# Kernel tuning notes

Measured on AMD Instinct MI355X. Metric: run time of the kernel, lower is better.

## Reference

```python
import jax, jax.numpy as jnp
import numpy as np

B, S, H, A = 64, 2048, 512, 512

def setup_inputs() -> dict:
    key = jax.random.key(0)
    k = jax.random.split(key, 8)
    s = 1.0 / np.sqrt(H)
    sa = 1.0 / np.sqrt(A)
    return {
        "decoder_output": jax.random.normal(k[0], (B, H), jnp.float32),
        "encoder_output": jax.random.normal(k[1], (B, S, H), jnp.float32),
        "W_dec": jax.random.uniform(k[2], (A, H), jnp.float32, -s, s),
        "b_dec": jax.random.uniform(k[3], (A,), jnp.float32, -s, s),
        "W_enc": jax.random.uniform(k[4], (A, H), jnp.float32, -s, s),
        "b_enc": jax.random.uniform(k[5], (A,), jnp.float32, -s, s),
        "V": jax.random.uniform(k[6], (1, A), jnp.float32, -sa, sa),
        "b_v": jax.random.uniform(k[7], (1,), jnp.float32, -sa, sa),
    }

def reference(decoder_output, encoder_output, W_dec, b_dec, W_enc, b_enc, V, b_v):
    # dec proj: (B, A); enc proj: (B, S, A)
    dec_p = decoder_output @ W_dec.T + b_dec
    enc_p = jnp.einsum('bsh,ah->bsa', encoder_output, W_enc) + b_enc
    h = jnp.tanh(dec_p[:, None, :] + enc_p)          # (B, S, A)
    scores = jnp.einsum('bsa,a->bs', h, V[0]) + b_v[0]  # (B, S)
    attn = jax.nn.softmax(scores, axis=-1)           # softmax over seq dim
    ctx = jnp.einsum('bs,bsh->bh', attn, encoder_output)  # (B, H)
    out = jnp.concatenate([ctx, decoder_output], axis=-1)  # (B, 2H)
    return out
```

## Files before the change

### kernel.cpp

```cpp
#include <hip/hip_runtime.h>
#include <cstdint>
#include <cstddef>

#define NB 64
#define NS 2048
#define NH 512
#define NA 512

#define BM 64
#define BK 32

typedef __attribute__((ext_vector_type(8))) short short8;
typedef __attribute__((ext_vector_type(4))) float f32x4;

__device__ inline short f2bf(float f) {
    union { float f; uint32_t u; } v; v.f = f;
    uint32_t u = v.u;
    uint32_t r = (u + 0x7fffu + ((u >> 16) & 1u)) >> 16;
    return (short)r;
}

__global__ __launch_bounds__(256) void k_decp(const float* __restrict__ dec,
                                              const float* __restrict__ Wd,
                                              const float* __restrict__ bd,
                                              const float* __restrict__ be,
                                              float* __restrict__ dp) {
    int b = blockIdx.x;
    __shared__ float dl[NH];
    for (int i = threadIdx.x; i < NH; i += 256) dl[i] = dec[b * NH + i];
    __syncthreads();
    for (int a = threadIdx.x; a < NA; a += 256) {
        const float4* wr = (const float4*)(Wd + (size_t)a * NH);
        float acc = 0.f;
#pragma unroll 8
        for (int h4 = 0; h4 < NH / 4; ++h4) {
            float4 w = wr[h4];
            acc += dl[h4*4+0]*w.x + dl[h4*4+1]*w.y + dl[h4*4+2]*w.z + dl[h4*4+3]*w.w;
        }
        dp[b * NA + a] = acc + bd[a] + be[a];
    }
}

__global__ __launch_bounds__(256) void k_packw(const float* __restrict__ We,
                                               short* __restrict__ wsw) {
    int t = blockIdx.x * 256 + threadIdx.x;
    int slot = t & 3;
    int a = (t >> 2) & (NA - 1);
    int kt = t >> 11;
    const float* src = We + (size_t)a * NH + kt * 32 + slot * 8;
    int dslot = slot ^ ((a >> 1) & 3);
    short* dst = wsw + (((size_t)kt * NA + a) * 4 + dslot) * 8;
    short8 o;
#pragma unroll
    for (int j = 0; j < 8; ++j) o[j] = f2bf(src[j]);
    *(short8*)dst = o;
}

__global__ __launch_bounds__(256, 2) void k_scores(const float* __restrict__ enc,
                                                   const short* __restrict__ wsw,
                                                   const float* __restrict__ dp,
                                                   const float* __restrict__ V,
                                                   float* __restrict__ scores) {
    __shared__ short Wl[NA * BK];
    __shared__ short Al[BM * BK];
    __shared__ float sbuf[4][BM];

    const int tid = threadIdx.x;
    const int w = tid >> 6;
    const int l = tid & 63;
    const int lrow = l & 15;
    const int lg = l >> 4;
    const int row0 = blockIdx.x * BM;
    const int b = row0 / NS;

    const int sa = tid >> 2;
    const int qa = tid & 3;
    const float* encp = enc + (size_t)(row0 + sa) * NH + qa * 8;
    short* awr = Al + ((size_t)sa * 4 + (qa ^ ((sa >> 1) & 3))) * 8;

    const char* wsrc = (const char*)wsw;

    f32x4 acc[4][8];
#pragma unroll
    for (int i = 0; i < 4; ++i)
#pragma unroll
        for (int j = 0; j < 8; ++j) acc[i][j] = (f32x4){0.f, 0.f, 0.f, 0.f};

    for (int kt = 0; kt < NH / BK; ++kt) {
#pragma unroll
        for (int r = 0; r < 8; ++r) {
            int blk = r * 4 + w;
            __builtin_amdgcn_global_load_lds(
                (const __attribute__((address_space(1))) void*)(wsrc + ((size_t)kt * 32768 + ((size_t)blk * 64 + l) * 16)),
                (__attribute__((address_space(3))) void*)((char*)Wl + blk * 1024),
                16, 0, 0);
        }
        float4 f0 = *(const float4*)(encp);
        float4 f1 = *(const float4*)(encp + 4);
        short8 ab;
        ab[0] = f2bf(f0.x); ab[1] = f2bf(f0.y); ab[2] = f2bf(f0.z); ab[3] = f2bf(f0.w);
        ab[4] = f2bf(f1.x); ab[5] = f2bf(f1.y); ab[6] = f2bf(f1.z); ab[7] = f2bf(f1.w);
        *(short8*)awr = ab;
        encp += BK;
        __syncthreads();

        short8 af[4], bfr[8];
#pragma unroll
        for (int fm = 0; fm < 4; ++fm) {
            int row = fm * 16 + lrow;
            af[fm] = *(const short8*)(Al + ((size_t)row * 4 + (lg ^ ((row >> 1) & 3))) * 8);
        }
#pragma unroll
        for (int fn = 0; fn < 8; ++fn) {
            int arow = w * 128 + fn * 16 + lrow;
            bfr[fn] = *(const short8*)(Wl + ((size_t)arow * 4 + (lg ^ ((arow >> 1) & 3))) * 8);
        }
#pragma unroll
        for (int fm = 0; fm < 4; ++fm)
#pragma unroll
            for (int fn = 0; fn < 8; ++fn)
                acc[fm][fn] = __builtin_amdgcn_mfma_f32_16x16x32_bf16(af[fm], bfr[fn], acc[fm][fn], 0, 0, 0);
        __syncthreads();
    }

    float dpl[8], vl[8];
#pragma unroll
    for (int fn = 0; fn < 8; ++fn) {
        int a = w * 128 + fn * 16 + lrow;
        dpl[fn] = dp[b * NA + a];
        vl[fn] = V[a];
    }
    float ps[4][4];
#pragma unroll
    for (int fm = 0; fm < 4; ++fm)
#pragma unroll
        for (int i = 0; i < 4; ++i) ps[fm][i] = 0.f;

#pragma unroll
    for (int fm = 0; fm < 4; ++fm)
#pragma unroll
        for (int fn = 0; fn < 8; ++fn)
#pragma unroll
            for (int i = 0; i < 4; ++i) {
                float x = acc[fm][fn][i] + dpl[fn];
                float u = exp2f(x * 2.885390082f);
                float th = 1.f - 2.f * __builtin_amdgcn_rcpf(u + 1.f);
                ps[fm][i] += th * vl[fn];
            }

#pragma unroll
    for (int fm = 0; fm < 4; ++fm)
#pragma unroll
        for (int i = 0; i < 4; ++i) {
            float v = ps[fm][i];
            v += __shfl_xor(v, 1);
            v += __shfl_xor(v, 2);
            v += __shfl_xor(v, 4);
            v += __shfl_xor(v, 8);
            if (lrow == 0) sbuf[w][fm * 16 + lg * 4 + i] = v;
        }
    __syncthreads();
    if (tid < BM) {
        float s = sbuf[0][tid] + sbuf[1][tid] + sbuf[2][tid] + sbuf[3][tid];
        scores[row0 + tid] = s;
    }
}

__global__ __launch_bounds__(256) void k_softmax(const float* __restrict__ scores,
                                                 float* __restrict__ attn) {
    int b = blockIdx.x;
    int tid = threadIdx.x;
    int l = tid & 63;
    int w = tid >> 6;
    const float4* src = (const float4*)(scores + (size_t)b * NS);
    float4 v0 = src[tid];
    float4 v1 = src[tid + 256];
    __shared__ float redm[4];
    __shared__ float reds[4];
    float m = fmaxf(fmaxf(fmaxf(v0.x, v0.y), fmaxf(v0.z, v0.w)),
                    fmaxf(fmaxf(v1.x, v1.y), fmaxf(v1.z, v1.w)));
#pragma unroll
    for (int off = 1; off < 64; off <<= 1) m = fmaxf(m, __shfl_xor(m, off));
    if (l == 0) redm[w] = m;
    __syncthreads();
    m = fmaxf(fmaxf(redm[0], redm[1]), fmaxf(redm[2], redm[3]));
    const float c = 1.4426950408889634f;
    float e[8];
    e[0] = exp2f((v0.x - m) * c); e[1] = exp2f((v0.y - m) * c);
    e[2] = exp2f((v0.z - m) * c); e[3] = exp2f((v0.w - m) * c);
    e[4] = exp2f((v1.x - m) * c); e[5] = exp2f((v1.y - m) * c);
    e[6] = exp2f((v1.z - m) * c); e[7] = exp2f((v1.w - m) * c);
    float s = e[0] + e[1] + e[2] + e[3] + e[4] + e[5] + e[6] + e[7];
#pragma unroll
    for (int off = 1; off < 64; off <<= 1) s += __shfl_xor(s, off);
    if (l == 0) reds[w] = s;
    __syncthreads();
    s = reds[0] + reds[1] + reds[2] + reds[3];
    float inv = 1.f / s;
    float4 o0 = { e[0]*inv, e[1]*inv, e[2]*inv, e[3]*inv };
    float4 o1 = { e[4]*inv, e[5]*inv, e[6]*inv, e[7]*inv };
    float4* dst = (float4*)(attn + (size_t)b * NS);
    dst[tid] = o0;
    dst[tid + 256] = o1;
}

__global__ __launch_bounds__(512) void k_ctx(const float* __restrict__ enc,
                                             const float* __restrict__ attn,
                                             const float* __restrict__ dec,
                                             float* __restrict__ out) {
    int b = blockIdx.x >> 2;
    int c = blockIdx.x & 3;
    int tid = threadIdx.x;
    __shared__ float al[NS];
    __shared__ float sb[512];
    ((float4*)al)[tid] = ((const float4*)(attn + (size_t)b * NS))[tid];
    __syncthreads();
    int h = c * 128 + (tid & 127);
    int sq = tid >> 7;
    const float* ep = enc + (size_t)b * NS * NH + (size_t)(sq * 512) * NH + h;
    float acc = 0.f;
#pragma unroll 8
    for (int s = 0; s < 512; ++s) {
        acc += al[sq * 512 + s] * ep[(size_t)s * NH];
    }
    sb[tid] = acc;
    __syncthreads();
    if (tid < 128) {
        float ctx = sb[tid] + sb[tid + 128] + sb[tid + 256] + sb[tid + 384];
        out[(size_t)b * 1024 + c * 128 + tid] = ctx;
        out[(size_t)b * 1024 + 512 + c * 128 + tid] = dec[(size_t)b * NH + c * 128 + tid];
    }
}

extern "C" void kernel_launch(void* const* d_in, const int* in_sizes, int n_in,
                              void* d_out, int out_size, void* d_ws, size_t ws_size,
                              hipStream_t stream) {
    (void)in_sizes; (void)n_in; (void)out_size; (void)ws_size;
    const float* dec = (const float*)d_in[0];
    const float* enc = (const float*)d_in[1];
    const float* Wd  = (const float*)d_in[2];
    const float* bd  = (const float*)d_in[3];
    const float* We  = (const float*)d_in[4];
    const float* be  = (const float*)d_in[5];
    const float* V   = (const float*)d_in[6];
    float* out = (float*)d_out;

    char* ws = (char*)d_ws;
    short* wsw    = (short*)ws;
    float* dpb    = (float*)(ws + 524288);
    float* scores = (float*)(ws + 524288 + 131072);
    float* attn   = (float*)(ws + 524288 + 131072 + 524288);

    k_decp<<<dim3(NB), dim3(256), 0, stream>>>(dec, Wd, bd, be, dpb);
    k_packw<<<dim3(128), dim3(256), 0, stream>>>(We, wsw);
    k_scores<<<dim3((NB * NS) / BM), dim3(256), 0, stream>>>(enc, wsw, dpb, V, scores);
    k_softmax<<<dim3(NB), dim3(256), 0, stream>>>(scores, attn);
    k_ctx<<<dim3(NB * 4), dim3(512), 0, stream>>>(enc, attn, dec, out);
}
```

Before: 192.9 us.

## Fuse scores, unnormalized softmax and context into one kernel with direct-register operands

Merges the score GEMM, exponentiation and partial context accumulation into a single kernel. Each 64-row tile computes exp(score) without max subtraction and writes a partial weighted sum of its encoder rows, so the encoder tensor is read once instead of twice. A small combine kernel then sums the partials and normalizes. The GEMM now loads A and W fragments straight from global memory into registers, using a packed bf16 convert instead of LDS staging and barriers. Skipping the max subtraction risks overflow when scores are large, and the direct loads give up LDS reuse of W across waves.

```diff
diff --git a/kernel.cpp b/kernel.cpp
--- a/kernel.cpp
+++ b/kernel.cpp
@@ -18,6 +18,12 @@
     uint32_t u = v.u;
     uint32_t r = (u + 0x7fffu + ((u >> 16) & 1u)) >> 16;
     return (short)r;
+}
+
+__device__ inline uint32_t cvtpk_bf16(float lo, float hi) {
+    uint32_t r;
+    asm("v_cvt_pk_bf16_f32 %0, %1, %2" : "=v"(r) : "v"(lo), "v"(hi));
+    return r;
 }
 
 __global__ __launch_bounds__(256) void k_decp(const float* __restrict__ dec,
@@ -48,22 +54,22 @@
     int a = (t >> 2) & (NA - 1);
     int kt = t >> 11;
     const float* src = We + (size_t)a * NH + kt * 32 + slot * 8;
-    int dslot = slot ^ ((a >> 1) & 3);
-    short* dst = wsw + (((size_t)kt * NA + a) * 4 + dslot) * 8;
+    short* dst = wsw + (((size_t)kt * NA + a) * 4 + slot) * 8;
     short8 o;
 #pragma unroll
     for (int j = 0; j < 8; ++j) o[j] = f2bf(src[j]);
     *(short8*)dst = o;
 }
 
-__global__ __launch_bounds__(256, 2) void k_scores(const float* __restrict__ enc,
-                                                   const short* __restrict__ wsw,
-                                                   const float* __restrict__ dp,
-                                                   const float* __restrict__ V,
-                                                   float* __restrict__ scores) {
-    __shared__ short Wl[NA * BK];
-    __shared__ short Al[BM * BK];
+__global__ __launch_bounds__(256, 2) void k_fused(const float* __restrict__ enc,
+                                                  const short* __restrict__ wsw,
+                                                  const float* __restrict__ dp,
+                                                  const float* __restrict__ V,
+                                                  float* __restrict__ pbuf,
+                                                  float* __restrict__ ctxp) {
     __shared__ float sbuf[4][BM];
+    __shared__ float pl[BM];
+    __shared__ float sb2[4][NH];
 
     const int tid = threadIdx.x;
     const int w = tid >> 6;
@@ -73,12 +79,8 @@
     const int row0 = blockIdx.x * BM;
     const int b = row0 / NS;
 
-    const int sa = tid >> 2;
-    const int qa = tid & 3;
-    const float* encp = enc + (size_t)(row0 + sa) * NH + qa * 8;
-    short* awr = Al + ((size_t)sa * 4 + (qa ^ ((sa >> 1) & 3))) * 8;
-
-    const char* wsrc = (const char*)wsw;
+    const float* ap = enc + (size_t)(row0 + lrow) * NH + lg * 8;
+    const short* bp = wsw + ((size_t)(w * 128 + lrow) * 4 + lg) * 8;
 
     f32x4 acc[4][8];
 #pragma unroll
@@ -86,41 +88,32 @@
 #pragma unroll
         for (int j = 0; j < 8; ++j) acc[i][j] = (f32x4){0.f, 0.f, 0.f, 0.f};
 
+#pragma unroll 2
     for (int kt = 0; kt < NH / BK; ++kt) {
-#pragma unroll
-        for (int r = 0; r < 8; ++r) {
-            int blk = r * 4 + w;
-            __builtin_amdgcn_global_load_lds(
-                (const __attribute__((address_space(1))) void*)(wsrc + ((size_t)kt * 32768 + ((size_t)blk * 64 + l) * 16)),
-                (__attribute__((address_space(3))) void*)((char*)Wl + blk * 1024),
-                16, 0, 0);
+        short8 bfr[8];
+#pragma unroll
+        for (int fn = 0; fn < 8; ++fn)
+            bfr[fn] = *(const short8*)(bp + (size_t)kt * 16384 + fn * 512);
+
+        short8 af[4];
+#pragma unroll
+        for (int fm = 0; fm < 4; ++fm) {
+            const float* a_ = ap + (size_t)kt * 32 + fm * (16 * NH);
+            f32x4 a0 = *(const f32x4*)(a_);
+            f32x4 a1 = *(const f32x4*)(a_ + 4);
+            union { short8 s8; uint32_t u[4]; } uu;
+            uu.u[0] = cvtpk_bf16(a0[0], a0[1]);
+            uu.u[1] = cvtpk_bf16(a0[2], a0[3]);
+            uu.u[2] = cvtpk_bf16(a1[0], a1[1]);
+            uu.u[3] = cvtpk_bf16(a1[2], a1[3]);
+            af[fm] = uu.s8;
         }
-        float4 f0 = *(const float4*)(encp);
-        float4 f1 = *(const float4*)(encp + 4);
-        short8 ab;
-        ab[0] = f2bf(f0.x); ab[1] = f2bf(f0.y); ab[2] = f2bf(f0.z); ab[3] = f2bf(f0.w);
-        ab[4] = f2bf(f1.x); ab[5] = f2bf(f1.y); ab[6] = f2bf(f1.z); ab[7] = f2bf(f1.w);
-        *(short8*)awr = ab;
-        encp += BK;
-        __syncthreads();
-
-        short8 af[4], bfr[8];
-#pragma unroll
-        for (int fm = 0; fm < 4; ++fm) {
-            int row = fm * 16 + lrow;
-            af[fm] = *(const short8*)(Al + ((size_t)row * 4 + (lg ^ ((row >> 1) & 3))) * 8);
-        }
-#pragma unroll
-        for (int fn = 0; fn < 8; ++fn) {
-            int arow = w * 128 + fn * 16 + lrow;
-            bfr[fn] = *(const short8*)(Wl + ((size_t)arow * 4 + (lg ^ ((arow >> 1) & 3))) * 8);
-        }
+
 #pragma unroll
         for (int fm = 0; fm < 4; ++fm)
 #pragma unroll
             for (int fn = 0; fn < 8; ++fn)
                 acc[fm][fn] = __builtin_amdgcn_mfma_f32_16x16x32_bf16(af[fm], bfr[fn], acc[fm][fn], 0, 0, 0);
-        __syncthreads();
     }
 
     float dpl[8], vl[8];
@@ -160,76 +153,74 @@
             if (lrow == 0) sbuf[w][fm * 16 + lg * 4 + i] = v;
         }
     __syncthreads();
+
     if (tid < BM) {
         float s = sbuf[0][tid] + sbuf[1][tid] + sbuf[2][tid] + sbuf[3][tid];
-        scores[row0 + tid] = s;
-    }
-}
-
-__global__ __launch_bounds__(256) void k_softmax(const float* __restrict__ scores,
-                                                 float* __restrict__ attn) {
+        float p = exp2f(s * 1.4426950408889634f);
+        pl[tid] = p;
+        pbuf[row0 + tid] = p;
+    }
+    __syncthreads();
+
+    f32x4 c0 = (f32x4){0.f, 0.f, 0.f, 0.f};
+    f32x4 c1 = (f32x4){0.f, 0.f, 0.f, 0.f};
+    const float* erow = enc + (size_t)(row0 + w * 16) * NH + l * 8;
+#pragma unroll 4
+    for (int s16 = 0; s16 < 16; ++s16) {
+        float pw = pl[w * 16 + s16];
+        f32x4 e0 = *(const f32x4*)(erow);
+        f32x4 e1 = *(const f32x4*)(erow + 4);
+        c0 += pw * e0;
+        c1 += pw * e1;
+        erow += NH;
+    }
+    *(f32x4*)(&sb2[w][l * 8]) = c0;
+    *(f32x4*)(&sb2[w][l * 8 + 4]) = c1;
+    __syncthreads();
+
+    {
+        int h2 = tid * 2;
+        float r0 = sb2[0][h2] + sb2[1][h2] + sb2[2][h2] + sb2[3][h2];
+        float r1 = sb2[0][h2+1] + sb2[1][h2+1] + sb2[2][h2+1] + sb2[3][h2+1];
+        float2* dst = (float2*)(ctxp + (size_t)blockIdx.x * NH + h2);
+        *dst = make_float2(r0, r1);
+    }
+}
+
+__global__ __launch_bounds__(256) void k_combine(const float* __restrict__ ctxp,
+                                                 const float* __restrict__ pbuf,
+                                                 const float* __restrict__ dec,
+                                                 float* __restrict__ out) {
     int b = blockIdx.x;
     int tid = threadIdx.x;
     int l = tid & 63;
     int w = tid >> 6;
-    const float4* src = (const float4*)(scores + (size_t)b * NS);
-    float4 v0 = src[tid];
-    float4 v1 = src[tid + 256];
-    __shared__ float redm[4];
-    __shared__ float reds[4];
-    float m = fmaxf(fmaxf(fmaxf(v0.x, v0.y), fmaxf(v0.z, v0.w)),
-                    fmaxf(fmaxf(v1.x, v1.y), fmaxf(v1.z, v1.w)));
-#pragma unroll
-    for (int off = 1; off < 64; off <<= 1) m = fmaxf(m, __shfl_xor(m, off));
-    if (l == 0) redm[w] = m;
-    __syncthreads();
-    m = fmaxf(fmaxf(redm[0], redm[1]), fmaxf(redm[2], redm[3]));
-    const float c = 1.4426950408889634f;
-    float e[8];
-    e[0] = exp2f((v0.x - m) * c); e[1] = exp2f((v0.y - m) * c);
-    e[2] = exp2f((v0.z - m) * c); e[3] = exp2f((v0.w - m) * c);
-    e[4] = exp2f((v1.x - m) * c); e[5] = exp2f((v1.y - m) * c);
-    e[6] = exp2f((v1.z - m) * c); e[7] = exp2f((v1.w - m) * c);
-    float s = e[0] + e[1] + e[2] + e[3] + e[4] + e[5] + e[6] + e[7];
+    __shared__ float red[4];
+    __shared__ float stot;
+
+    const f32x4* pv = (const f32x4*)(pbuf + (size_t)b * NS);
+    f32x4 v0 = pv[tid * 2];
+    f32x4 v1 = pv[tid * 2 + 1];
+    float s = v0[0]+v0[1]+v0[2]+v0[3]+v1[0]+v1[1]+v1[2]+v1[3];
 #pragma unroll
     for (int off = 1; off < 64; off <<= 1) s += __shfl_xor(s, off);
-    if (l == 0) reds[w] = s;
-    __syncthreads();
-    s = reds[0] + reds[1] + reds[2] + reds[3];
-    float inv = 1.f / s;
-    float4 o0 = { e[0]*inv, e[1]*inv, e[2]*inv, e[3]*inv };
-    float4 o1 = { e[4]*inv, e[5]*inv, e[6]*inv, e[7]*inv };
-    float4* dst = (float4*)(attn + (size_t)b * NS);
-    dst[tid] = o0;
-    dst[tid + 256] = o1;
-}
-
-__global__ __launch_bounds__(512) void k_ctx(const float* __restrict__ enc,
-                                             const float* __restrict__ attn,
-                                             const float* __restrict__ dec,
-                                             float* __restrict__ out) {
-    int b = blockIdx.x >> 2;
-    int c = blockIdx.x & 3;
-    int tid = threadIdx.x;
-    __shared__ float al[NS];
-    __shared__ float sb[512];
-    ((float4*)al)[tid] = ((const float4*)(attn + (size_t)b * NS))[tid];
-    __syncthreads();
-    int h = c * 128 + (tid & 127);
-    int sq = tid >> 7;
-    const float* ep = enc + (size_t)b * NS * NH + (size_t)(sq * 512) * NH + h;
-    float acc = 0.f;
+    if (l == 0) red[w] = s;
+    __syncthreads();
+    if (tid == 0) stot = red[0] + red[1] + red[2] + red[3];
+    __syncthreads();
+    float inv = 1.f / stot;
+
+    int h2 = tid * 2;
+    float a0 = 0.f, a1 = 0.f;
 #pragma unroll 8
-    for (int s = 0; s < 512; ++s) {
-        acc += al[sq * 512 + s] * ep[(size_t)s * NH];
-    }
-    sb[tid] = acc;
-    __syncthreads();
-    if (tid < 128) {
-        float ctx = sb[tid] + sb[tid + 128] + sb[tid + 256] + sb[tid + 384];
-        out[(size_t)b * 1024 + c * 128 + tid] = ctx;
-        out[(size_t)b * 1024 + 512 + c * 128 + tid] = dec[(size_t)b * NH + c * 128 + tid];
-    }
+    for (int i = 0; i < NS / BM; ++i) {
+        const float2 c = *(const float2*)(ctxp + ((size_t)b * (NS / BM) + i) * NH + h2);
+        a0 += c.x;
+        a1 += c.y;
+    }
+    *(float2*)(out + (size_t)b * 1024 + h2) = make_float2(a0 * inv, a1 * inv);
+    const float2 dv = *(const float2*)(dec + (size_t)b * NH + h2);
+    *(float2*)(out + (size_t)b * 1024 + NH + h2) = dv;
 }
 
 extern "C" void kernel_launch(void* const* d_in, const int* in_sizes, int n_in,
@@ -247,13 +238,12 @@
 
     char* ws = (char*)d_ws;
     short* wsw    = (short*)ws;
-    float* dpb    = (float*)(ws + 524288);
-    float* scores = (float*)(ws + 524288 + 131072);
-    float* attn   = (float*)(ws + 524288 + 131072 + 524288);
+    float* dpb    = (float*)(ws + (512 << 10));
+    float* pbuf   = (float*)(ws + (640 << 10));
+    float* ctxp   = (float*)(ws + (1152 << 10));
 
     k_decp<<<dim3(NB), dim3(256), 0, stream>>>(dec, Wd, bd, be, dpb);
     k_packw<<<dim3(128), dim3(256), 0, stream>>>(We, wsw);
-    k_scores<<<dim3((NB * NS) / BM), dim3(256), 0, stream>>>(enc, wsw, dpb, V, scores);
-    k_softmax<<<dim3(NB), dim3(256), 0, stream>>>(scores, attn);
-    k_ctx<<<dim3(NB * 4), dim3(512), 0, stream>>>(enc, attn, dec, out);
-}
+    k_fused<<<dim3((NB * NS) / BM), dim3(256), 0, stream>>>(enc, wsw, dpb, V, pbuf, ctxp);
+    k_combine<<<dim3(NB), dim3(256), 0, stream>>>(ctxp, pbuf, dec, out);
+}
```

After: 260.9 us. +35.3%, slower.
